# Kernel optimization log

Measured on AMD Instinct MI355X. Metric: run time of the kernel, lower is better.

Reference implementation:

```python
import jax, jax.numpy as jnp
import numpy as np

N_QUBITS = 11   # state dim 2**11 = 2048
N_LAYERS = 6
BATCH = 8192


def _rz(phi):
    # RZ(phi) = diag(e^{-i phi/2}, e^{+i phi/2}); phi scalar -> (2,2), phi (B,) -> (B,2,2)
    e = jnp.exp(-0.5j * phi.astype(jnp.complex64))
    z = jnp.zeros_like(e)
    return jnp.stack([jnp.stack([e, z], -1), jnp.stack([z, jnp.conj(e)], -1)], -2)


def _ry(theta):
    # RY(theta) = [[cos t, -sin t], [sin t, cos t]], t = theta/2
    t = 0.5 * theta.astype(jnp.float32)
    c = jnp.cos(t).astype(jnp.complex64)
    s = jnp.sin(t).astype(jnp.complex64)
    return jnp.stack([jnp.stack([c, -s], -1), jnp.stack([s, c], -1)], -2)


def _apply_1q(state, U, q, n):
    # state: (B, 2**n); qubit q is the q-th most-significant bit of the ket index
    B = state.shape[0]
    st = state.reshape(B, 2 ** q, 2, 2 ** (n - 1 - q))
    if U.ndim == 2:   # shared (trainable) gate
        st = jnp.einsum('ab,sxby->sxay', U, st)
    else:             # per-sample (data-encoding) gate, U: (B,2,2)
        st = jnp.einsum('sab,sxby->sxay', U, st)
    return st.reshape(B, 2 ** n)


def _apply_cnot(state, c, n):
    # CNOT with control c, target c+1 (adjacent in the chain)
    B = state.shape[0]
    st = state.reshape(B, 2 ** c, 2, 2, 2 ** (n - 2 - c))
    st = jnp.stack([st[:, :, 0], st[:, :, 1, ::-1]], axis=2)  # flip target when control=1
    return st.reshape(B, 2 ** n)


def _forward(X, params):
    n, L = N_QUBITS, N_LAYERS
    B = X.shape[0]
    # pad/truncate features to n_qubits (matches build_circuit)
    Xe = X[:, :n] if X.shape[1] >= n else jnp.pad(X, ((0, 0), (0, n - X.shape[1])))
    state = jnp.zeros((B, 2 ** n), jnp.complex64).at[:, 0].set(1.0)  # |0...0>
    for l in range(L):
        for q in range(n):
            state = _apply_1q(state, _rz(params[l, q, 0]), q, n)
            state = _apply_1q(state, _ry(params[l, q, 1]), q, n)
            state = _apply_1q(state, _rz(params[l, q, 2]), q, n)
            if l == L - 1:  # data re-upload RY only on the last layer (per source)
                state = _apply_1q(state, _ry(Xe[:, q]), q, n)
        if n > 1:
            for c in range(n - 1):
                state = _apply_cnot(state, c, n)
    return state  # (B, 2**n) complex64


def setup_inputs() -> dict:
    key = jax.random.key(0)
    k1, k2 = jax.random.split(key)
    X = jax.random.uniform(k1, (BATCH, N_QUBITS), jnp.float32) * (2.0 * np.pi)
    params = jax.random.normal(k2, (N_LAYERS, N_QUBITS, 3), jnp.float32) * 0.01
    return {"X": X, "params": params}


def reference(X, params):
    state = _forward(X, params)
    # return real/imag stacked so the output is a real float32 array
    return jnp.stack([state.real, state.imag], -1)  # (B, 2**n, 2)
```

## Files before the change

### kernel.cpp

```cpp
#include <hip/hip_runtime.h>
#include <math.h>

#define NQ   11
#define DIM  2048
#define NL   6

__host__ __device__ constexpr int swzA(int x) {
    return x ^ ((x >> 6) & 31) ^ ((x & 2) << 3) ^ ((x & 1) << 3);
}
__host__ __device__ constexpr int swzB(int x) {
    return x ^ ((x >> 7) & 7) ^ ((x >> 3) & 14) ^ ((x >> 6) & 8);
}

__device__ __forceinline__ float2 cfma2(float2 u, float2 a, float2 v, float2 b) {
    float2 r;
    r.x = u.x*a.x - u.y*a.y + v.x*b.x - v.y*b.y;
    r.y = u.x*a.y + u.y*a.x + v.x*b.y + v.y*b.x;
    return r;
}

__global__ __launch_bounds__(256) void qnn_shared_kernel(
    const float* __restrict__ P,
    float2* __restrict__ ws)
{
    __shared__ float2 lds[DIM];
    __shared__ float2 G[NL*NQ][4];
    const int t = threadIdx.x;

    if (t < NL*NQ) {
        const float p0 = P[t*3+0], p1 = P[t*3+1], p2 = P[t*3+2];
        const float th = 0.5f*p1;
        const float c  = cosf(th), s = sinf(th);
        const float al = 0.5f*(p0+p2), be = 0.5f*(p0-p2);
        const float ca = cosf(al), sa = sinf(al);
        const float cb = cosf(be), sb = sinf(be);
        G[t][0] = make_float2( c*ca, -c*sa);
        G[t][1] = make_float2(-s*cb, -s*sb);
        G[t][2] = make_float2( s*cb, -s*sb);
        G[t][3] = make_float2( c*ca,  c*sa);
    }

    const int a0w = swzA(t);
    const int a1b = swzA(((t>>5)<<8) | (t&31));
    const int a2b = swzA(((t>>2)<<5) | (t&3));
    const int a3b = swzA(t ^ (t>>1));
    const int natb = ((t>>2)<<5) | (t&3);

    float2 a[8];
    #pragma unroll
    for (int k = 0; k < 8; ++k) a[k] = make_float2(0.f, 0.f);
    if (t == 0) a[0] = make_float2(1.f, 0.f);
    __syncthreads();

    #define CG(g_, rb_) { \
        const float2 U00=G[g_][0], U01=G[g_][1], U10=G[g_][2], U11=G[g_][3]; \
        _Pragma("unroll") \
        for (int kk = 0; kk < 8; ++kk) if (!(kk & (rb_))) { \
            const float2 a0 = a[kk], a1 = a[kk|(rb_)]; \
            a[kk]       = cfma2(U00, a0, U01, a1); \
            a[kk|(rb_)] = cfma2(U10, a0, U11, a1); \
        } }

    #define SG(g_, m_, b_) { \
        const float2 ca_ = (b_) ? G[g_][3] : G[g_][0]; \
        const float2 cb_ = (b_) ? G[g_][2] : G[g_][1]; \
        _Pragma("unroll") \
        for (int kk = 0; kk < 8; ++kk) { \
            float2 p; \
            p.x = __shfl_xor(a[kk].x, m_); \
            p.y = __shfl_xor(a[kk].y, m_); \
            a[kk] = cfma2(ca_, a[kk], cb_, p); \
        } }

    for (int l = 0; l < NL; ++l) {
        const int g0 = l*NQ;
        CG(g0+0, 4) CG(g0+1, 2) CG(g0+2, 1)

        #pragma unroll
        for (int k = 0; k < 8; ++k) lds[a0w ^ swzA(k<<8)] = a[k];
        __syncthreads();
        #pragma unroll
        for (int k = 0; k < 8; ++k) a[k] = lds[a1b ^ swzA(k<<5)];
        __syncthreads();
        CG(g0+3, 4) CG(g0+4, 2) CG(g0+5, 1)

        #pragma unroll
        for (int k = 0; k < 8; ++k) lds[a1b ^ swzA(k<<5)] = a[k];
        __syncthreads();
        #pragma unroll
        for (int k = 0; k < 8; ++k) a[k] = lds[a2b ^ swzA(k<<2)];
        __syncthreads();
        CG(g0+6, 4) CG(g0+7, 2) CG(g0+8, 1)

        SG(g0+9, 2, (t>>1)&1)
        SG(g0+10, 1, t&1)

        if (l < NL-1) {
            #pragma unroll
            for (int k = 0; k < 8; ++k) lds[a2b ^ swzA(k<<2)] = a[k];
            __syncthreads();
            #pragma unroll
            for (int k = 0; k < 8; ++k)
                a[k] = lds[a3b ^ swzA((k<<8) ^ (k<<7))];
            __syncthreads();
        } else {
            #pragma unroll
            for (int k = 0; k < 8; ++k) ws[natb | (k<<2)] = a[k];
        }
    }
    #undef CG
    #undef SG
}

__global__ __launch_bounds__(128, 4) void qnn_last_kernel(
    const float* __restrict__ X,
    const float2* __restrict__ S5,
    float2* __restrict__ out)
{
    __shared__ float2 lds[DIM];
    __shared__ float2 gc[NQ];
    const int b = blockIdx.x;
    const int t = threadIdx.x;

    if (t < NQ) {
        const float tx = 0.5f * X[(size_t)b*NQ + t];
        gc[t] = make_float2(cosf(tx), sinf(tx));
    }

    const int b0 = swzB(t);
    const int b1 = swzB(((t>>3)<<7) | (t&7));
    const int b2 = swzB(t<<4);
    const int b3 = swzB(t ^ (t>>1));

    float2 a[16];
    #pragma unroll
    for (int k = 0; k < 16; ++k) a[k] = S5[(k<<7) | t];
    __syncthreads();

    #define RG(q_, rb_) { \
        const float c = gc[q_].x, s = gc[q_].y; \
        _Pragma("unroll") \
        for (int kk = 0; kk < 16; ++kk) if (!(kk & (rb_))) { \
            const float2 a0 = a[kk], a1 = a[kk|(rb_)]; \
            float2 n0, n1; \
            n0.x = fmaf(c, a0.x, -s*a1.x); \
            n0.y = fmaf(c, a0.y, -s*a1.y); \
            n1.x = fmaf(s, a0.x,  c*a1.x); \
            n1.y = fmaf(s, a0.y,  c*a1.y); \
            a[kk] = n0; a[kk|(rb_)] = n1; \
        } }

    RG(0, 8) RG(1, 4) RG(2, 2) RG(3, 1)

    #pragma unroll
    for (int k = 0; k < 16; ++k) lds[b0 ^ swzB(k<<7)] = a[k];
    __syncthreads();
    #pragma unroll
    for (int k = 0; k < 16; ++k) a[k] = lds[b1 ^ swzB(k<<3)];
    __syncthreads();
    RG(4, 8) RG(5, 4) RG(6, 2) RG(7, 1)

    #pragma unroll
    for (int k = 0; k < 16; ++k) lds[b1 ^ swzB(k<<3)] = a[k];
    __syncthreads();
    #pragma unroll
    for (int k = 0; k < 16; ++k) a[k] = lds[b2 ^ swzB(k)];
    __syncthreads();
    RG(8, 4) RG(9, 2) RG(10, 1)

    #pragma unroll
    for (int k = 0; k < 16; ++k) lds[b2 ^ swzB(k)] = a[k];
    __syncthreads();
    float2* o = out + (size_t)b * DIM + t;
    #pragma unroll
    for (int k = 0; k < 16; ++k)
        o[k<<7] = lds[b3 ^ swzB((k<<7) ^ (k<<6))];
    #undef RG
}

extern "C" void kernel_launch(void* const* d_in, const int* in_sizes, int n_in,
                              void* d_out, int out_size, void* d_ws, size_t ws_size,
                              hipStream_t stream) {
    const float* X = (const float*)d_in[0];
    const float* P = (const float*)d_in[1];
    float2* out = (float2*)d_out;
    float2* ws  = (float2*)d_ws;
    const int B = in_sizes[0] / NQ;
    qnn_shared_kernel<<<1, 256, 0, stream>>>(P, ws);
    qnn_last_kernel<<<B, 128, 0, stream>>>(X, ws, out);
}
```

Baseline: 52.76 us.

## Use 256-thread blocks with shuffle gates and packed float2 math in last-layer kernel

```diff
diff --git a/kernel.cpp b/kernel.cpp
--- a/kernel.cpp
+++ b/kernel.cpp
@@ -5,26 +5,25 @@
 #define DIM  2048
 #define NL   6
 
+typedef float v2f __attribute__((ext_vector_type(2)));
+
 __host__ __device__ constexpr int swzA(int x) {
     return x ^ ((x >> 6) & 31) ^ ((x & 2) << 3) ^ ((x & 1) << 3);
 }
-__host__ __device__ constexpr int swzB(int x) {
-    return x ^ ((x >> 7) & 7) ^ ((x >> 3) & 14) ^ ((x >> 6) & 8);
-}
-
-__device__ __forceinline__ float2 cfma2(float2 u, float2 a, float2 v, float2 b) {
-    float2 r;
-    r.x = u.x*a.x - u.y*a.y + v.x*b.x - v.y*b.y;
-    r.y = u.x*a.y + u.y*a.x + v.x*b.y + v.y*b.x;
-    return r;
+
+__device__ __forceinline__ v2f cmadd(v2f u, v2f a, v2f acc) {
+    v2f ap; ap.x = -a.y; ap.y = a.x;
+    acc += u.x * a;
+    acc += u.y * ap;
+    return acc;
 }
 
 __global__ __launch_bounds__(256) void qnn_shared_kernel(
     const float* __restrict__ P,
-    float2* __restrict__ ws)
+    v2f* __restrict__ ws)
 {
-    __shared__ float2 lds[DIM];
-    __shared__ float2 G[NL*NQ][4];
+    __shared__ v2f lds[DIM];
+    __shared__ v2f G[NL*NQ][4];
     const int t = threadIdx.x;
 
     if (t < NL*NQ) {
@@ -34,10 +33,10 @@
         const float al = 0.5f*(p0+p2), be = 0.5f*(p0-p2);
         const float ca = cosf(al), sa = sinf(al);
         const float cb = cosf(be), sb = sinf(be);
-        G[t][0] = make_float2( c*ca, -c*sa);
-        G[t][1] = make_float2(-s*cb, -s*sb);
-        G[t][2] = make_float2( s*cb, -s*sb);
-        G[t][3] = make_float2( c*ca,  c*sa);
+        G[t][0] = (v2f){ c*ca, -c*sa};
+        G[t][1] = (v2f){-s*cb, -s*sb};
+        G[t][2] = (v2f){ s*cb, -s*sb};
+        G[t][3] = (v2f){ c*ca,  c*sa};
     }
 
     const int a0w = swzA(t);
@@ -46,30 +45,30 @@
     const int a3b = swzA(t ^ (t>>1));
     const int natb = ((t>>2)<<5) | (t&3);
 
-    float2 a[8];
-    #pragma unroll
-    for (int k = 0; k < 8; ++k) a[k] = make_float2(0.f, 0.f);
-    if (t == 0) a[0] = make_float2(1.f, 0.f);
+    v2f a[8];
+    #pragma unroll
+    for (int k = 0; k < 8; ++k) a[k] = (v2f){0.f, 0.f};
+    if (t == 0) a[0] = (v2f){1.f, 0.f};
     __syncthreads();
 
     #define CG(g_, rb_) { \
-        const float2 U00=G[g_][0], U01=G[g_][1], U10=G[g_][2], U11=G[g_][3]; \
+        const v2f U00=G[g_][0], U01=G[g_][1], U10=G[g_][2], U11=G[g_][3]; \
         _Pragma("unroll") \
         for (int kk = 0; kk < 8; ++kk) if (!(kk & (rb_))) { \
-            const float2 a0 = a[kk], a1 = a[kk|(rb_)]; \
-            a[kk]       = cfma2(U00, a0, U01, a1); \
-            a[kk|(rb_)] = cfma2(U10, a0, U11, a1); \
+            const v2f a0 = a[kk], a1 = a[kk|(rb_)]; \
+            a[kk]       = cmadd(U01, a1, cmadd(U00, a0, (v2f){0.f,0.f})); \
+            a[kk|(rb_)] = cmadd(U11, a1, cmadd(U10, a0, (v2f){0.f,0.f})); \
         } }
 
     #define SG(g_, m_, b_) { \
-        const float2 ca_ = (b_) ? G[g_][3] : G[g_][0]; \
-        const float2 cb_ = (b_) ? G[g_][2] : G[g_][1]; \
+        const v2f ca_ = (b_) ? G[g_][3] : G[g_][0]; \
+        const v2f cb_ = (b_) ? G[g_][2] : G[g_][1]; \
         _Pragma("unroll") \
         for (int kk = 0; kk < 8; ++kk) { \
-            float2 p; \
+            v2f p; \
             p.x = __shfl_xor(a[kk].x, m_); \
             p.y = __shfl_xor(a[kk].y, m_); \
-            a[kk] = cfma2(ca_, a[kk], cb_, p); \
+            a[kk] = cmadd(cb_, p, cmadd(ca_, a[kk], (v2f){0.f,0.f})); \
         } }
 
     for (int l = 0; l < NL; ++l) {
@@ -112,70 +111,81 @@
     #undef SG
 }
 
-__global__ __launch_bounds__(128, 4) void qnn_last_kernel(
+__global__ __launch_bounds__(256, 8) void qnn_last_kernel(
     const float* __restrict__ X,
-    const float2* __restrict__ S5,
-    float2* __restrict__ out)
+    const v2f* __restrict__ S5,
+    v2f* __restrict__ out)
 {
-    __shared__ float2 lds[DIM];
-    __shared__ float2 gc[NQ];
+    __shared__ v2f lds[DIM];
+    __shared__ v2f gc[NQ];
     const int b = blockIdx.x;
     const int t = threadIdx.x;
 
     if (t < NQ) {
         const float tx = 0.5f * X[(size_t)b*NQ + t];
-        gc[t] = make_float2(cosf(tx), sinf(tx));
+        gc[t] = (v2f){cosf(tx), sinf(tx)};
     }
 
-    const int b0 = swzB(t);
-    const int b1 = swzB(((t>>3)<<7) | (t&7));
-    const int b2 = swzB(t<<4);
-    const int b3 = swzB(t ^ (t>>1));
-
-    float2 a[16];
-    #pragma unroll
-    for (int k = 0; k < 16; ++k) a[k] = S5[(k<<7) | t];
+    const int a0w = swzA(t);
+    const int a1b = swzA(((t>>5)<<8) | (t&31));
+    const int a2b = swzA(((t>>2)<<5) | (t&3));
+    const int a3b = swzA(t ^ (t>>1));
+
+    v2f a[8];
+    #pragma unroll
+    for (int k = 0; k < 8; ++k) a[k] = S5[(k<<8) | t];
     __syncthreads();
 
     #define RG(q_, rb_) { \
         const float c = gc[q_].x, s = gc[q_].y; \
         _Pragma("unroll") \
-        for (int kk = 0; kk < 16; ++kk) if (!(kk & (rb_))) { \
-            const float2 a0 = a[kk], a1 = a[kk|(rb_)]; \
-            float2 n0, n1; \
-            n0.x = fmaf(c, a0.x, -s*a1.x); \
-            n0.y = fmaf(c, a0.y, -s*a1.y); \
-            n1.x = fmaf(s, a0.x,  c*a1.x); \
-            n1.y = fmaf(s, a0.y,  c*a1.y); \
-            a[kk] = n0; a[kk|(rb_)] = n1; \
-        } }
-
-    RG(0, 8) RG(1, 4) RG(2, 2) RG(3, 1)
-
-    #pragma unroll
-    for (int k = 0; k < 16; ++k) lds[b0 ^ swzB(k<<7)] = a[k];
-    __syncthreads();
-    #pragma unroll
-    for (int k = 0; k < 16; ++k) a[k] = lds[b1 ^ swzB(k<<3)];
-    __syncthreads();
-    RG(4, 8) RG(5, 4) RG(6, 2) RG(7, 1)
-
-    #pragma unroll
-    for (int k = 0; k < 16; ++k) lds[b1 ^ swzB(k<<3)] = a[k];
-    __syncthreads();
-    #pragma unroll
-    for (int k = 0; k < 16; ++k) a[k] = lds[b2 ^ swzB(k)];
-    __syncthreads();
-    RG(8, 4) RG(9, 2) RG(10, 1)
-
-    #pragma unroll
-    for (int k = 0; k < 16; ++k) lds[b2 ^ swzB(k)] = a[k];
-    __syncthreads();
-    float2* o = out + (size_t)b * DIM + t;
-    #pragma unroll
-    for (int k = 0; k < 16; ++k)
-        o[k<<7] = lds[b3 ^ swzB((k<<7) ^ (k<<6))];
+        for (int kk = 0; kk < 8; ++kk) if (!(kk & (rb_))) { \
+            const v2f a0 = a[kk], a1 = a[kk|(rb_)]; \
+            a[kk]       = c*a0 - s*a1; \
+            a[kk|(rb_)] = s*a0 + c*a1; \
+        } }
+
+    #define LG(q_, m_, bit_) { \
+        const float c = gc[q_].x, s = gc[q_].y; \
+        const float sg = (bit_) ? s : -s; \
+        _Pragma("unroll") \
+        for (int kk = 0; kk < 8; ++kk) { \
+            v2f p; \
+            p.x = __shfl_xor(a[kk].x, m_); \
+            p.y = __shfl_xor(a[kk].y, m_); \
+            a[kk] = c*a[kk] + sg*p; \
+        } }
+
+    RG(0, 4) RG(1, 2) RG(2, 1)
+
+    #pragma unroll
+    for (int k = 0; k < 8; ++k) lds[a0w ^ swzA(k<<8)] = a[k];
+    __syncthreads();
+    #pragma unroll
+    for (int k = 0; k < 8; ++k) a[k] = lds[a1b ^ swzA(k<<5)];
+    __syncthreads();
+    RG(3, 4) RG(4, 2) RG(5, 1)
+
+    #pragma unroll
+    for (int k = 0; k < 8; ++k) lds[a1b ^ swzA(k<<5)] = a[k];
+    __syncthreads();
+    #pragma unroll
+    for (int k = 0; k < 8; ++k) a[k] = lds[a2b ^ swzA(k<<2)];
+    __syncthreads();
+    RG(6, 4) RG(7, 2) RG(8, 1)
+
+    LG(9, 2, (t>>1)&1)
+    LG(10, 1, t&1)
+
+    #pragma unroll
+    for (int k = 0; k < 8; ++k) lds[a2b ^ swzA(k<<2)] = a[k];
+    __syncthreads();
+    v2f* o = out + (size_t)b * DIM + t;
+    #pragma unroll
+    for (int k = 0; k < 8; ++k)
+        o[k<<8] = lds[a3b ^ swzA((k<<8) ^ (k<<7))];
     #undef RG
+    #undef LG
 }
 
 extern "C" void kernel_launch(void* const* d_in, const int* in_sizes, int n_in,
@@ -183,9 +193,9 @@
                               hipStream_t stream) {
     const float* X = (const float*)d_in[0];
     const float* P = (const float*)d_in[1];
-    float2* out = (float2*)d_out;
-    float2* ws  = (float2*)d_ws;
+    v2f* out = (v2f*)d_out;
+    v2f* ws  = (v2f*)d_ws;
     const int B = in_sizes[0] / NQ;
     qnn_shared_kernel<<<1, 256, 0, stream>>>(P, ws);
-    qnn_last_kernel<<<B, 128, 0, stream>>>(X, ws, out);
-}
+    qnn_last_kernel<<<B, 256, 0, stream>>>(X, ws, out);
+}
```

Result: slower. 56.61 us (+7.3%).

## Map each batch sample to one wavefront using register shuffles instead of LDS

Applied to the files above, without the earlier changes.

```diff
diff --git a/kernel.cpp b/kernel.cpp
--- a/kernel.cpp
+++ b/kernel.cpp
@@ -5,11 +5,10 @@
 #define DIM  2048
 #define NL   6
 
+typedef float v2f __attribute__((ext_vector_type(2)));
+
 __host__ __device__ constexpr int swzA(int x) {
     return x ^ ((x >> 6) & 31) ^ ((x & 2) << 3) ^ ((x & 1) << 3);
-}
-__host__ __device__ constexpr int swzB(int x) {
-    return x ^ ((x >> 7) & 7) ^ ((x >> 3) & 14) ^ ((x >> 6) & 8);
 }
 
 __device__ __forceinline__ float2 cfma2(float2 u, float2 a, float2 v, float2 b) {
@@ -112,70 +111,64 @@
     #undef SG
 }
 
-__global__ __launch_bounds__(128, 4) void qnn_last_kernel(
+__global__ __launch_bounds__(256, 4) void qnn_last_kernel(
     const float* __restrict__ X,
     const float2* __restrict__ S5,
     float2* __restrict__ out)
 {
-    __shared__ float2 lds[DIM];
-    __shared__ float2 gc[NQ];
-    const int b = blockIdx.x;
-    const int t = threadIdx.x;
+    const int lane = threadIdx.x & 63;
+    const int wid  = threadIdx.x >> 6;
+    const int b    = blockIdx.x * 4 + wid;
 
-    if (t < NQ) {
-        const float tx = 0.5f * X[(size_t)b*NQ + t];
-        gc[t] = make_float2(cosf(tx), sinf(tx));
+    float vc = 1.f, vs = 0.f;
+    if (lane < NQ) {
+        const float tx = 0.5f * X[(size_t)b*NQ + lane];
+        vc = cosf(tx); vs = sinf(tx);
     }
 
-    const int b0 = swzB(t);
-    const int b1 = swzB(((t>>3)<<7) | (t&7));
-    const int b2 = swzB(t<<4);
-    const int b3 = swzB(t ^ (t>>1));
-
-    float2 a[16];
+    v2f a[32];
     #pragma unroll
-    for (int k = 0; k < 16; ++k) a[k] = S5[(k<<7) | t];
-    __syncthreads();
+    for (int k = 0; k < 32; ++k) {
+        const float2 t = S5[(k<<6) | lane];
+        a[k] = (v2f){t.x, t.y};
+    }
 
     #define RG(q_, rb_) { \
-        const float c = gc[q_].x, s = gc[q_].y; \
+        const float c = __shfl(vc, q_), s = __shfl(vs, q_); \
         _Pragma("unroll") \
-        for (int kk = 0; kk < 16; ++kk) if (!(kk & (rb_))) { \
-            const float2 a0 = a[kk], a1 = a[kk|(rb_)]; \
-            float2 n0, n1; \
-            n0.x = fmaf(c, a0.x, -s*a1.x); \
-            n0.y = fmaf(c, a0.y, -s*a1.y); \
-            n1.x = fmaf(s, a0.x,  c*a1.x); \
-            n1.y = fmaf(s, a0.y,  c*a1.y); \
-            a[kk] = n0; a[kk|(rb_)] = n1; \
+        for (int kk = 0; kk < 32; ++kk) if (!(kk & (rb_))) { \
+            const v2f a0 = a[kk], a1 = a[kk|(rb_)]; \
+            a[kk]       = c*a0 - s*a1; \
+            a[kk|(rb_)] = s*a0 + c*a1; \
         } }
 
-    RG(0, 8) RG(1, 4) RG(2, 2) RG(3, 1)
+    #define LG(q_, m_) { \
+        const float c = __shfl(vc, q_), s = __shfl(vs, q_); \
+        const float sg = (lane & (m_)) ? s : -s; \
+        _Pragma("unroll") \
+        for (int kk = 0; kk < 32; ++kk) { \
+            v2f p; \
+            p.x = __shfl_xor(a[kk].x, m_); \
+            p.y = __shfl_xor(a[kk].y, m_); \
+            a[kk] = c*a[kk] + sg*p; \
+        } }
 
+    RG(0,16) RG(1,8) RG(2,4) RG(3,2) RG(4,1)
+    LG(5,32) LG(6,16) LG(7,8) LG(8,4) LG(9,2) LG(10,1)
+
+    const int i0 = lane ^ (lane >> 1);
+    const int i1 = i0 ^ 32;
+    float2* o = out + (size_t)b * DIM + lane;
     #pragma unroll
-    for (int k = 0; k < 16; ++k) lds[b0 ^ swzB(k<<7)] = a[k];
-    __syncthreads();
-    #pragma unroll
-    for (int k = 0; k < 16; ++k) a[k] = lds[b1 ^ swzB(k<<3)];
-    __syncthreads();
-    RG(4, 8) RG(5, 4) RG(6, 2) RG(7, 1)
-
-    #pragma unroll
-    for (int k = 0; k < 16; ++k) lds[b1 ^ swzB(k<<3)] = a[k];
-    __syncthreads();
-    #pragma unroll
-    for (int k = 0; k < 16; ++k) a[k] = lds[b2 ^ swzB(k)];
-    __syncthreads();
-    RG(8, 4) RG(9, 2) RG(10, 1)
-
-    #pragma unroll
-    for (int k = 0; k < 16; ++k) lds[b2 ^ swzB(k)] = a[k];
-    __syncthreads();
-    float2* o = out + (size_t)b * DIM + t;
-    #pragma unroll
-    for (int k = 0; k < 16; ++k)
-        o[k<<7] = lds[b3 ^ swzB((k<<7) ^ (k<<6))];
+    for (int k = 0; k < 32; ++k) {
+        const int sk = k ^ (k >> 1);
+        float2 v;
+        v.x = __shfl(a[sk].x, (k & 1) ? i1 : i0);
+        v.y = __shfl(a[sk].y, (k & 1) ? i1 : i0);
+        o[k<<6] = v;
+    }
     #undef RG
+    #undef LG
 }
 
 extern "C" void kernel_launch(void* const* d_in, const int* in_sizes, int n_in,
@@ -187,5 +180,5 @@
     float2* ws  = (float2*)d_ws;
     const int B = in_sizes[0] / NQ;
     qnn_shared_kernel<<<1, 256, 0, stream>>>(P, ws);
-    qnn_last_kernel<<<B, 128, 0, stream>>>(X, ws, out);
+    qnn_last_kernel<<<B/4, 256, 0, stream>>>(X, ws, out);
 }
```

Result: slower. 69.66 us (+32.0%).

## Replace final LDS round-trip with DPP lane exchanges for last three qubits

Applied to the files above, without the earlier changes.

```diff
diff --git a/kernel.cpp b/kernel.cpp
--- a/kernel.cpp
+++ b/kernel.cpp
@@ -4,6 +4,8 @@
 #define NQ   11
 #define DIM  2048
 #define NL   6
+
+typedef float v2f __attribute__((ext_vector_type(2)));
 
 __host__ __device__ constexpr int swzA(int x) {
     return x ^ ((x >> 6) & 31) ^ ((x & 2) << 3) ^ ((x & 1) << 3);
@@ -16,6 +18,16 @@
     float2 r;
     r.x = u.x*a.x - u.y*a.y + v.x*b.x - v.y*b.y;
     r.y = u.x*a.y + u.y*a.x + v.x*b.y + v.y*b.x;
+    return r;
+}
+
+template<int CTRL>
+__device__ __forceinline__ v2f dpp_xor(v2f v) {
+    const int x = __builtin_amdgcn_update_dpp(
+        0, __float_as_int(v.x), CTRL, 0xF, 0xF, true);
+    const int y = __builtin_amdgcn_update_dpp(
+        0, __float_as_int(v.y), CTRL, 0xF, 0xF, true);
+    v2f r; r.x = __int_as_float(x); r.y = __int_as_float(y);
     return r;
 }
 
@@ -129,53 +141,67 @@
 
     const int b0 = swzB(t);
     const int b1 = swzB(((t>>3)<<7) | (t&7));
-    const int b2 = swzB(t<<4);
     const int b3 = swzB(t ^ (t>>1));
 
-    float2 a[16];
-    #pragma unroll
-    for (int k = 0; k < 16; ++k) a[k] = S5[(k<<7) | t];
+    v2f a[16];
+    #pragma unroll
+    for (int k = 0; k < 16; ++k) {
+        const float2 v = S5[(k<<7) | t];
+        a[k] = (v2f){v.x, v.y};
+    }
     __syncthreads();
 
     #define RG(q_, rb_) { \
         const float c = gc[q_].x, s = gc[q_].y; \
         _Pragma("unroll") \
         for (int kk = 0; kk < 16; ++kk) if (!(kk & (rb_))) { \
-            const float2 a0 = a[kk], a1 = a[kk|(rb_)]; \
-            float2 n0, n1; \
-            n0.x = fmaf(c, a0.x, -s*a1.x); \
-            n0.y = fmaf(c, a0.y, -s*a1.y); \
-            n1.x = fmaf(s, a0.x,  c*a1.x); \
-            n1.y = fmaf(s, a0.y,  c*a1.y); \
-            a[kk] = n0; a[kk|(rb_)] = n1; \
+            const v2f a0 = a[kk], a1 = a[kk|(rb_)]; \
+            a[kk]       = c*a0 - s*a1; \
+            a[kk|(rb_)] = s*a0 + c*a1; \
+        } }
+
+    #define LGD(q_, CTRL_, r_) { \
+        const float c = gc[q_].x, s = gc[q_].y; \
+        const float sg = (r_) ? s : -s; \
+        _Pragma("unroll") \
+        for (int kk = 0; kk < 16; ++kk) { \
+            const v2f p = dpp_xor<CTRL_>(a[kk]); \
+            a[kk] = c*a[kk] + sg*p; \
         } }
 
     RG(0, 8) RG(1, 4) RG(2, 2) RG(3, 1)
 
     #pragma unroll
-    for (int k = 0; k < 16; ++k) lds[b0 ^ swzB(k<<7)] = a[k];
-    __syncthreads();
-    #pragma unroll
-    for (int k = 0; k < 16; ++k) a[k] = lds[b1 ^ swzB(k<<3)];
-    __syncthreads();
+    for (int k = 0; k < 16; ++k)
+        lds[b0 ^ swzB(k<<7)] = make_float2(a[k].x, a[k].y);
+    __syncthreads();
+    #pragma unroll
+    for (int k = 0; k < 16; ++k) {
+        const float2 v = lds[b1 ^ swzB(k<<3)];
+        a[k] = (v2f){v.x, v.y};
+    }
     RG(4, 8) RG(5, 4) RG(6, 2) RG(7, 1)
 
     #pragma unroll
-    for (int k = 0; k < 16; ++k) lds[b1 ^ swzB(k<<3)] = a[k];
-    __syncthreads();
-    #pragma unroll
-    for (int k = 0; k < 16; ++k) a[k] = lds[b2 ^ swzB(k)];
-    __syncthreads();
-    RG(8, 4) RG(9, 2) RG(10, 1)
-
-    #pragma unroll
-    for (int k = 0; k < 16; ++k) lds[b2 ^ swzB(k)] = a[k];
-    __syncthreads();
+    for (int k = 0; k < 16; ++k)
+        lds[b1 ^ swzB(k<<3)] = make_float2(a[k].x, a[k].y);
+    __syncthreads();
+    #pragma unroll
+    for (int k = 0; k < 16; ++k) {
+        const float2 v = lds[b3 ^ swzB((k<<7) ^ (k<<6))];
+        a[k] = (v2f){v.x, v.y};
+    }
+
+    LGD(8, 0x141, ((t>>2) ^ (t>>3)) & 1)
+    LGD(9, 27,    ((t>>1) ^ (t>>2)) & 1)
+    LGD(10, 177,  ( t     ^ (t>>1)) & 1)
+
     float2* o = out + (size_t)b * DIM + t;
     #pragma unroll
     for (int k = 0; k < 16; ++k)
-        o[k<<7] = lds[b3 ^ swzB((k<<7) ^ (k<<6))];
+        o[k<<7] = make_float2(a[k].x, a[k].y);
     #undef RG
+    #undef LGD
 }
 
 extern "C" void kernel_launch(void* const* d_in, const int* in_sizes, int n_in,
```

New measurement: 52.46 us. About the same (-0.6%).
